# Performance work log

Hardware: AMD Instinct MI355X
Metric: run time of the kernel (lower is better)

Reference implementation:

```python
import jax, jax.numpy as jnp
import numpy as np

B, S, D = 4, 2048, 2048
H, HD = 16, 128
ROPE_THETA = 10000.0


def rotate_half(x):
    half = x.shape[-1] // 2
    return jnp.concatenate([-x[..., half:], x[..., :half]], axis=-1)


def setup_inputs() -> dict:
    key = jax.random.key(0)
    ks = jax.random.split(key, 5)
    scale = 1.0 / np.sqrt(D)
    x = jax.random.normal(ks[0], (B, S, D), dtype=jnp.float32)
    wq = jax.random.normal(ks[1], (D, H * HD), dtype=jnp.float32) * scale
    wk = jax.random.normal(ks[2], (D, H * HD), dtype=jnp.float32) * scale
    wv = jax.random.normal(ks[3], (D, H * HD), dtype=jnp.float32) * scale
    wo = jax.random.normal(ks[4], (H * HD, D), dtype=jnp.float32) * scale
    # RoPE frequencies: freqs_cis real/imag parts, shape [S, HD//2]
    inv_freq = 1.0 / (ROPE_THETA ** (np.arange(0, HD, 2, dtype=np.float32) / HD))
    t = np.arange(S, dtype=np.float32)
    freqs = np.outer(t, inv_freq)  # [S, HD//2]
    cos = jnp.asarray(np.cos(freqs), dtype=jnp.float32)
    sin = jnp.asarray(np.sin(freqs), dtype=jnp.float32)
    return {"x": x, "wq": wq, "wk": wk, "wv": wv, "wo": wo, "cos": cos, "sin": sin}


def reference(x, wq, wk, wv, wo, cos, sin):
    batch, seq_len, _ = x.shape
    # QKV projections (no bias), reshape to [b, h, s, d]
    q = (x @ wq).reshape(batch, seq_len, H, HD).transpose(0, 2, 1, 3)
    k = (x @ wk).reshape(batch, seq_len, H, HD).transpose(0, 2, 1, 3)
    v = (x @ wv).reshape(batch, seq_len, H, HD)  # [b, s, h, d]
    # RoPE (half-split / rotate_half convention)
    cos_full = jnp.concatenate([cos, cos], axis=-1)[None, None, :seq_len, :]
    sin_full = jnp.concatenate([sin, sin], axis=-1)[None, None, :seq_len, :]
    q = q * cos_full + rotate_half(q) * sin_full
    k = k * cos_full + rotate_half(k) * sin_full
    # Scaled dot-product attention with causal mask
    logits = jnp.einsum('bhqd,bhkd->bhqk', q, k) / jnp.sqrt(jnp.float32(HD))
    causal = jnp.tril(jnp.ones((seq_len, seq_len), dtype=bool))
    logits = jnp.where(causal[None, None, :, :], logits, -1e10)
    weights = jax.nn.softmax(logits, axis=-1)
    out = jnp.einsum('bhqk,bkhd->bqhd', weights, v)
    out = out.reshape(batch, seq_len, H * HD)
    return out @ wo
```

## Files before the change

### kernel.cpp

```cpp
#include <hip/hip_runtime.h>
#include <cstdint>
#include <cstddef>

typedef unsigned short u16;
using bf16x8  = __attribute__((ext_vector_type(8))) short;
using floatx4 = __attribute__((ext_vector_type(4))) float;

__device__ __forceinline__ u16 f2bf(float f) {
    union { float f; unsigned u; } v; v.f = f;
    unsigned r = v.u + 0x7fffu + ((v.u >> 16) & 1u);
    return (u16)(r >> 16);
}
__device__ __forceinline__ float bf2f(u16 h) {
    union { unsigned u; float f; } v; v.u = ((unsigned)h) << 16; return v.f;
}
__device__ __forceinline__ floatx4 mfma16(bf16x8 a, bf16x8 b, floatx4 c) {
    return __builtin_amdgcn_mfma_f32_16x16x32_bf16(a, b, c, 0, 0, 0);
}
using gptr_t = const __attribute__((address_space(1))) unsigned int*;
using lptr_t = __attribute__((address_space(3))) unsigned int*;
__device__ __forceinline__ void lds16(const void* g, void* l) {
    __builtin_amdgcn_global_load_lds((gptr_t)g, (lptr_t)l, 16, 0, 0);
}
typedef __attribute__((address_space(3))) const u16* lds_cp;
__device__ __forceinline__ bf16x8 dsr128(const u16* p) {
    bf16x8 r;
    asm volatile("ds_read_b128 %0, %1" : "=v"(r) : "v"((lds_cp)p));
    return r;
}

#define ATT_SCALE 0.1275758218522532f

__global__ __launch_bounds__(256) void cvt_x(const float* __restrict__ x, u16* __restrict__ xb) {
    size_t i = ((size_t)blockIdx.x * 256 + threadIdx.x) * 4;
    float4 v = *(const float4*)&x[i];
    ushort4 r; r.x = f2bf(v.x); r.y = f2bf(v.y); r.z = f2bf(v.z); r.w = f2bf(v.w);
    *(ushort4*)&xb[i] = r;
}

__global__ __launch_bounds__(256) void transpose_wall(const float* __restrict__ wq, const float* __restrict__ wk,
                                                      const float* __restrict__ wv, const float* __restrict__ wo,
                                                      u16* __restrict__ wqkvb, u16* __restrict__ wob) {
    __shared__ float t[64][65];
    const int z = blockIdx.z;
    const float* in = (z == 0) ? wq : (z == 1) ? wk : (z == 2) ? wv : wo;
    u16* out = (z < 3) ? (wqkvb + (size_t)z * 2048 * 2048) : wob;
    int k0 = blockIdx.x * 64, n0 = blockIdx.y * 64;
    int tx = threadIdx.x, ty = threadIdx.y;
#pragma unroll
    for (int i = 0; i < 16; ++i) {
        int r = i * 4 + ty;
        t[r][tx] = in[(size_t)(k0 + r) * 2048 + n0 + tx];
    }
    __syncthreads();
#pragma unroll
    for (int i = 0; i < 16; ++i) {
        int r = i * 4 + ty;
        out[(size_t)(n0 + r) * 2048 + k0 + tx] = f2bf(t[tx][r]);
    }
}

template <int MODE>
__global__ __launch_bounds__(512, 2) void gemm_bt(const u16* __restrict__ A, const u16* __restrict__ B,
                                                  u16* __restrict__ Qo, u16* __restrict__ Ko, u16* __restrict__ Vt,
                                                  float* __restrict__ Co,
                                                  const float* __restrict__ cosb, const float* __restrict__ sinb) {
    __shared__ __align__(16) u16 sA[2][16384];
    __shared__ __align__(16) u16 sB[2][16384];

    const int nbx = (MODE == 0) ? 24 : 8;
    const int bid = blockIdx.x;
    const int q8 = (int)gridDim.x >> 3;
    const int wg = (bid & 7) * q8 + (bid >> 3);
    const int bx = wg % nbx, by = wg / nbx;
    const int m0 = by << 8, n0 = bx << 8;

    const int tid = threadIdx.x;
    const int w = tid >> 6, lane = tid & 63;
    const int wm = w >> 2, wn = w & 3;
    const int m16 = lane & 15, q4 = lane >> 4;
    const int lr = lane >> 3;
    const int lc8 = (lane & 7) ^ lr;
    const int wnbase = (wn >> 1) * 128 + (wn & 1) * 32;

    const u16* Ag = A + (size_t)(m0 + w * 16 + lr) * 2048 + lc8 * 8;
    const u16* Bg = B + (size_t)(n0 + w * 16 + lr) * 2048 + lc8 * 8;

    const int swz0 = ((q4 ^ (m16 & 7)) << 3);
    const int swz1 = (((4 + q4) ^ (m16 & 7)) << 3);

    floatx4 acc[8][4];
#pragma unroll
    for (int r = 0; r < 8; ++r)
#pragma unroll
        for (int c = 0; c < 4; ++c) acc[r][c] = (floatx4)0.0f;
    bf16x8 af[4][2];
    bf16x8 bf[4][2];

#define STAGE_A(b, h, t) do { \
    lds16(Ag + (size_t)((h) * 128) * 2048 + (t) * 64,     &sA[b][(h) * 8192 + w * 1024]);       \
    lds16(Ag + (size_t)((h) * 128 + 8) * 2048 + (t) * 64, &sA[b][(h) * 8192 + w * 1024 + 512]); \
} while (0)
#define STAGE_B(b, h, t) do { \
    lds16(Bg + (size_t)((h) * 128) * 2048 + (t) * 64,     &sB[b][(h) * 8192 + w * 1024]);       \
    lds16(Bg + (size_t)((h) * 128 + 8) * 2048 + (t) * 64, &sB[b][(h) * 8192 + w * 1024 + 512]); \
} while (0)
#define BAR() __builtin_amdgcn_s_barrier()
#define WAITL0() do { asm volatile("s_waitcnt lgkmcnt(0)" ::: "memory"); __builtin_amdgcn_sched_barrier(0); } while (0)
#define WAITL8() asm volatile("s_waitcnt lgkmcnt(8)" ::: "memory")
#define LDA_(cur, mq) do { _Pragma("unroll") for (int fr = 0; fr < 4; ++fr) { \
    const u16* p = &sA[cur][(wm * 128 + (mq) * 64 + fr * 16 + m16) * 64];      \
    af[fr][0] = dsr128(&p[swz0]);                                              \
    af[fr][1] = dsr128(&p[swz1]); } } while (0)
#define LDB_(cur, nq) do { _Pragma("unroll") for (int c = 0; c < 2; ++c) {     \
    const int j = (nq) * 2 + c;                                                \
    const u16* p = &sB[cur][(wnbase + (j & 1) * 16 + (j >> 1) * 64 + m16) * 64]; \
    bf[j][0] = dsr128(&p[swz0]);                                               \
    bf[j][1] = dsr128(&p[swz1]); } } while (0)
#define MM_(mq, nq) do { _Pragma("unroll") for (int kk = 0; kk < 2; ++kk)      \
    _Pragma("unroll") for (int fr = 0; fr < 4; ++fr)                           \
    _Pragma("unroll") for (int c = 0; c < 2; ++c)                              \
        acc[(mq) * 4 + fr][(nq) * 2 + c] =                                     \
            mfma16(af[fr][kk], bf[(nq) * 2 + c][kk], acc[(mq) * 4 + fr][(nq) * 2 + c]); } while (0)

    const int NT = 32;

    STAGE_B(0, 0, 0); STAGE_B(0, 1, 0);
    STAGE_A(0, 0, 0); STAGE_A(0, 1, 0);
    STAGE_B(1, 0, 1); STAGE_B(1, 1, 1);
    asm volatile("s_waitcnt vmcnt(4)" ::: "memory");
    __builtin_amdgcn_s_barrier();

#pragma unroll 2
    for (int t = 0; t < NT; ++t) {
        const int cur = t & 1;
        LDB_(cur, 0);
        LDA_(cur, 0);
        if (t + 1 < NT) STAGE_A(cur ^ 1, 0, t + 1);
        WAITL8();
        BAR();
        WAITL0();
        __builtin_amdgcn_s_setprio(1); MM_(0, 0); __builtin_amdgcn_s_setprio(0);
        BAR();
        LDB_(cur, 1);
        if (t + 1 < NT) STAGE_A(cur ^ 1, 1, t + 1);
        BAR();
        WAITL0();
        __builtin_amdgcn_s_setprio(1); MM_(0, 1); __builtin_amdgcn_s_setprio(0);
        BAR();
        LDA_(cur, 1);
        if (t + 2 < NT) STAGE_B(cur, 0, t + 2);
        BAR();
        WAITL0();
        __builtin_amdgcn_s_setprio(1); MM_(1, 1); __builtin_amdgcn_s_setprio(0);
        BAR();
        if (t + 2 < NT) STAGE_B(cur, 1, t + 2);
        BAR();
        __builtin_amdgcn_s_setprio(1); MM_(1, 0); __builtin_amdgcn_s_setprio(0);
        if (t + 2 < NT)      { asm volatile("s_waitcnt vmcnt(4)" ::: "memory"); }
        else if (t + 1 < NT) { asm volatile("s_waitcnt vmcnt(0)" ::: "memory"); }
        BAR();
    }

#undef STAGE_A
#undef STAGE_B
#undef BAR
#undef WAITL0
#undef WAITL8
#undef LDA_
#undef LDB_
#undef MM_

    if (MODE == 0) {
        const int which = n0 >> 11;
        if (which < 2) {
            u16* dst = (which == 0) ? Qo : Ko;
            const float sc = (which == 0) ? ATT_SCALE : 1.0f;
            const int h = ((n0 >> 7) + (wn >> 1)) & 15;
            const int dp0 = (wn & 1) * 32 + m16;
#pragma unroll
            for (int fr = 0; fr < 8; ++fr) {
                const int mb = m0 + wm * 128 + fr * 16 + q4 * 4;
#pragma unroll
                for (int c0 = 0; c0 < 2; ++c0) {
                    const int dp = dp0 + c0 * 16;
#pragma unroll
                    for (int i = 0; i < 4; ++i) {
                        const int mm = mb + i;
                        const int b = mm >> 11, s = mm & 2047;
                        const float cs = cosb[(size_t)s * 64 + dp];
                        const float sn = sinb[(size_t)s * 64 + dp];
                        const float lo = acc[fr][c0][i], hi = acc[fr][c0 + 2][i];
                        const size_t base = ((size_t)((b * 16 + h) * 2048 + s) << 7) + dp;
                        dst[base]      = f2bf((lo * cs - hi * sn) * sc);
                        dst[base + 64] = f2bf((hi * cs + lo * sn) * sc);
                    }
                }
            }
        } else {
#pragma unroll
            for (int fr = 0; fr < 8; ++fr) {
                const int mb = m0 + wm * 128 + fr * 16 + q4 * 4;
                const int b = mb >> 11, s = mb & 2047;
#pragma unroll
                for (int c = 0; c < 4; ++c) {
                    const int n = n0 + wnbase + (c & 1) * 16 + (c >> 1) * 64 + m16;
                    const int h = (n >> 7) & 15, d = n & 127;
                    ushort4 pk;
                    pk.x = f2bf(acc[fr][c][0]); pk.y = f2bf(acc[fr][c][1]);
                    pk.z = f2bf(acc[fr][c][2]); pk.w = f2bf(acc[fr][c][3]);
                    *(ushort4*)&Vt[((size_t)((b * 16 + h) * 128 + d)) * 2048 + s] = pk;
                }
            }
        }
    } else {
#pragma unroll
        for (int fr = 0; fr < 8; ++fr) {
            const int mb = m0 + wm * 128 + fr * 16 + q4 * 4;
#pragma unroll
            for (int c = 0; c < 4; ++c) {
                const int n = n0 + wnbase + (c & 1) * 16 + (c >> 1) * 64 + m16;
#pragma unroll
                for (int i = 0; i < 4; ++i)
                    Co[(size_t)(mb + i) * 2048 + n] = acc[fr][c][i];
            }
        }
    }
}

__global__ __launch_bounds__(512) void attn_kernel(const u16* __restrict__ Q, const u16* __restrict__ K,
                                                   const u16* __restrict__ VT, u16* __restrict__ AO) {
    __shared__ __align__(16) u16 ks[64 * 136];
    __shared__ __align__(16) u16 vts[128 * 72];
    __shared__ __align__(16) u16 ps[256 * 72];
    static const int iqmap[8] = {7, 6, 5, 4, 0, 1, 2, 3};
    const int bx = blockIdx.x;
    const int iq = iqmap[bx >> 6];
    const int bh = bx & 63;
    const int b = bh >> 4, h = bh & 15;
    const u16* Qg = Q  + (size_t)bh * (2048 * 128);
    const u16* Kg = K  + (size_t)bh * (2048 * 128);
    const u16* Vg = VT + (size_t)bh * (128 * 2048);
    const int tid = threadIdx.x, w = tid >> 6, lane = tid & 63;
    const int m16 = lane & 15, q4 = lane >> 4;
    const int jn = 4 * iq + 4;

    const int qrow = iq * 256 + w * 32;
    bf16x8 qf[2][4];
#pragma unroll
    for (int rm = 0; rm < 2; ++rm)
#pragma unroll
        for (int kk = 0; kk < 4; ++kk)
            qf[rm][kk] = *(const bf16x8*)&Qg[(size_t)(qrow + rm * 16 + m16) * 128 + kk * 32 + q4 * 8];

    floatx4 o[2][8];
#pragma unroll
    for (int rm = 0; rm < 2; ++rm)
#pragma unroll
        for (int c = 0; c < 8; ++c) o[rm][c] = (floatx4)0.0f;
    float mrow[2] = {-1e30f, -1e30f}, lrow[2] = {0.0f, 0.0f};

    const int kr0 = tid >> 4,          kc0 = tid & 15;
    const int kr1 = (512 + tid) >> 4,  kc1 = tid & 15;
    const int vr0 = tid >> 3,          vc0 = tid & 7;
    const int vr1 = (512 + tid) >> 3,  vc1 = tid & 7;
    uint4 kreg0, kreg1, vreg0, vreg1;

#define LOADKV(j) do { \
    kreg0 = *(const uint4*)&Kg[(size_t)((j) * 64 + kr0) * 128 + kc0 * 8]; \
    kreg1 = *(const uint4*)&Kg[(size_t)((j) * 64 + kr1) * 128 + kc1 * 8]; \
    vreg0 = *(const uint4*)&Vg[(size_t)vr0 * 2048 + (j) * 64 + vc0 * 8];  \
    vreg1 = *(const uint4*)&Vg[(size_t)vr1 * 2048 + (j) * 64 + vc1 * 8];  \
} while (0)

    LOADKV(0);

    for (int j = 0; j < jn; ++j) {
        asm volatile("" ::: "memory");
        __builtin_amdgcn_s_barrier();
        asm volatile("" ::: "memory");
        *(uint4*)&ks[kr0 * 136 + kc0 * 8] = kreg0;
        *(uint4*)&ks[kr1 * 136 + kc1 * 8] = kreg1;
        *(uint4*)&vts[vr0 * 72 + vc0 * 8] = vreg0;
        *(uint4*)&vts[vr1 * 72 + vc1 * 8] = vreg1;
        if (j + 1 < jn) LOADKV(j + 1);
        asm volatile("s_waitcnt lgkmcnt(0)" ::: "memory");
        __builtin_amdgcn_s_barrier();
        asm volatile("" ::: "memory");

        floatx4 sacc[2][4];
#pragma unroll
        for (int rm = 0; rm < 2; ++rm)
#pragma unroll
            for (int r = 0; r < 4; ++r) sacc[rm][r] = (floatx4)0.0f;
        __builtin_amdgcn_s_setprio(1);
#pragma unroll
        for (int kk = 0; kk < 4; ++kk) {
            bf16x8 kb[4];
#pragma unroll
            for (int r = 0; r < 4; ++r)
                kb[r] = *(const bf16x8*)&ks[(r * 16 + m16) * 136 + kk * 32 + q4 * 8];
#pragma unroll
            for (int rm = 0; rm < 2; ++rm)
#pragma unroll
                for (int r = 0; r < 4; ++r)
                    sacc[rm][r] = mfma16(kb[r], qf[rm][kk], sacc[rm][r]);
        }
        __builtin_amdgcn_s_setprio(0);

        if (j >= 4 * iq) {
#pragma unroll
            for (int rm = 0; rm < 2; ++rm) {
                const int qg = qrow + rm * 16 + m16;
#pragma unroll
                for (int r = 0; r < 4; ++r)
#pragma unroll
                    for (int i = 0; i < 4; ++i) {
                        int kg = j * 64 + r * 16 + q4 * 4 + i;
                        if (kg > qg) sacc[rm][r][i] = -1e30f;
                    }
            }
        }

#pragma unroll
        for (int rm = 0; rm < 2; ++rm) {
            float pmax = -1e30f;
#pragma unroll
            for (int r = 0; r < 4; ++r)
#pragma unroll
                for (int i = 0; i < 4; ++i) pmax = fmaxf(pmax, sacc[rm][r][i]);
            pmax = fmaxf(pmax, __shfl_xor(pmax, 16));
            pmax = fmaxf(pmax, __shfl_xor(pmax, 32));
            float mnew = fmaxf(mrow[rm], pmax);
            float alpha = __builtin_amdgcn_exp2f(mrow[rm] - mnew);
            mrow[rm] = mnew;

            float psum = 0.0f;
#pragma unroll
            for (int r = 0; r < 4; ++r) {
                float p0 = __builtin_amdgcn_exp2f(sacc[rm][r][0] - mnew);
                float p1 = __builtin_amdgcn_exp2f(sacc[rm][r][1] - mnew);
                float p2 = __builtin_amdgcn_exp2f(sacc[rm][r][2] - mnew);
                float p3 = __builtin_amdgcn_exp2f(sacc[rm][r][3] - mnew);
                psum += (p0 + p1) + (p2 + p3);
                ushort4 pk; pk.x = f2bf(p0); pk.y = f2bf(p1); pk.z = f2bf(p2); pk.w = f2bf(p3);
                *(ushort4*)&ps[(w * 32 + rm * 16 + m16) * 72 + r * 16 + q4 * 4] = pk;
            }
            psum += __shfl_xor(psum, 16);
            psum += __shfl_xor(psum, 32);
            lrow[rm] = lrow[rm] * alpha + psum;

            float abc[4];
#pragma unroll
            for (int i = 0; i < 4; ++i) abc[i] = __shfl(alpha, q4 * 4 + i);
#pragma unroll
            for (int c = 0; c < 8; ++c)
#pragma unroll
                for (int i = 0; i < 4; ++i) o[rm][c][i] *= abc[i];
        }

#pragma unroll
        for (int kk = 0; kk < 2; ++kk) {
            bf16x8 pa[2];
#pragma unroll
            for (int rm = 0; rm < 2; ++rm)
                pa[rm] = *(const bf16x8*)&ps[(w * 32 + rm * 16 + m16) * 72 + kk * 32 + q4 * 8];
            __builtin_amdgcn_s_setprio(1);
#pragma unroll
            for (int ch = 0; ch < 2; ++ch) {
                bf16x8 vb[4];
#pragma unroll
                for (int c = 0; c < 4; ++c)
                    vb[c] = *(const bf16x8*)&vts[((ch * 4 + c) * 16 + m16) * 72 + kk * 32 + q4 * 8];
#pragma unroll
                for (int rm = 0; rm < 2; ++rm)
#pragma unroll
                    for (int c = 0; c < 4; ++c)
                        o[rm][ch * 4 + c] = mfma16(pa[rm], vb[c], o[rm][ch * 4 + c]);
            }
            __builtin_amdgcn_s_setprio(0);
        }
    }
#undef LOADKV

#pragma unroll
    for (int rm = 0; rm < 2; ++rm) {
        float linv = __builtin_amdgcn_rcpf(lrow[rm]);
        float li[4];
#pragma unroll
        for (int i = 0; i < 4; ++i) li[i] = __shfl(linv, q4 * 4 + i);
#pragma unroll
        for (int c = 0; c < 8; ++c)
#pragma unroll
            for (int i = 0; i < 4; ++i) {
                int s = qrow + rm * 16 + q4 * 4 + i;
                int d = c * 16 + m16;
                AO[((size_t)(b * 2048 + s)) * 2048 + h * 128 + d] = f2bf(o[rm][c][i] * li[i]);
            }
    }
}

extern "C" void kernel_launch(void* const* d_in, const int* in_sizes, int n_in,
                              void* d_out, int out_size, void* d_ws, size_t ws_size,
                              hipStream_t stream) {
    const float* x    = (const float*)d_in[0];
    const float* wq   = (const float*)d_in[1];
    const float* wk   = (const float*)d_in[2];
    const float* wv   = (const float*)d_in[3];
    const float* wo   = (const float*)d_in[4];
    const float* cosb = (const float*)d_in[5];
    const float* sinb = (const float*)d_in[6];
    float* out = (float*)d_out;

    char* ws = (char*)d_ws;
    u16* xb    = (u16*)(ws);
    u16* AO    = xb;
    u16* wqkvb = (u16*)(ws + 33554432);
    u16* wob   = (u16*)(ws + 58720256);
    u16* Qb    = (u16*)(ws + 67108864);
    u16* Kb    = (u16*)(ws + 100663296);
    u16* Vtb   = (u16*)(ws + 134217728);

    cvt_x<<<16384, 256, 0, stream>>>(x, xb);
    transpose_wall<<<dim3(32, 32, 4), dim3(64, 4), 0, stream>>>(wq, wk, wv, wo, wqkvb, wob);

    gemm_bt<0><<<768, 512, 0, stream>>>(xb, wqkvb, Qb, Kb, Vtb, nullptr, cosb, sinb);
    attn_kernel<<<512, 512, 0, stream>>>(Qb, Kb, Vtb, AO);
    gemm_bt<1><<<256, 512, 0, stream>>>(AO, wob, nullptr, nullptr, nullptr, out, nullptr, nullptr);
}
```

Before: 548.2 us.

## Merge prep kernels, skip masked KV tiles per warp, lazily rescale softmax

```diff
diff --git a/kernel.cpp b/kernel.cpp
--- a/kernel.cpp
+++ b/kernel.cpp
@@ -31,32 +31,40 @@
 
 #define ATT_SCALE 0.1275758218522532f
 
-__global__ __launch_bounds__(256) void cvt_x(const float* __restrict__ x, u16* __restrict__ xb) {
-    size_t i = ((size_t)blockIdx.x * 256 + threadIdx.x) * 4;
-    float4 v = *(const float4*)&x[i];
-    ushort4 r; r.x = f2bf(v.x); r.y = f2bf(v.y); r.z = f2bf(v.z); r.w = f2bf(v.w);
-    *(ushort4*)&xb[i] = r;
-}
-
-__global__ __launch_bounds__(256) void transpose_wall(const float* __restrict__ wq, const float* __restrict__ wk,
-                                                      const float* __restrict__ wv, const float* __restrict__ wo,
-                                                      u16* __restrict__ wqkvb, u16* __restrict__ wob) {
-    __shared__ float t[64][65];
+__global__ __launch_bounds__(256) void prep(const float* __restrict__ x,
+                                            const float* __restrict__ wq, const float* __restrict__ wk,
+                                            const float* __restrict__ wv, const float* __restrict__ wo,
+                                            u16* __restrict__ xb,
+                                            u16* __restrict__ wqkvb, u16* __restrict__ wob) {
     const int z = blockIdx.z;
-    const float* in = (z == 0) ? wq : (z == 1) ? wk : (z == 2) ? wv : wo;
-    u16* out = (z < 3) ? (wqkvb + (size_t)z * 2048 * 2048) : wob;
-    int k0 = blockIdx.x * 64, n0 = blockIdx.y * 64;
-    int tx = threadIdx.x, ty = threadIdx.y;
-#pragma unroll
-    for (int i = 0; i < 16; ++i) {
-        int r = i * 4 + ty;
-        t[r][tx] = in[(size_t)(k0 + r) * 2048 + n0 + tx];
-    }
-    __syncthreads();
-#pragma unroll
-    for (int i = 0; i < 16; ++i) {
-        int r = i * 4 + ty;
-        out[(size_t)(n0 + r) * 2048 + k0 + tx] = f2bf(t[tx][r]);
+    const int tx = threadIdx.x, ty = threadIdx.y;
+    if (z < 4) {
+        __shared__ float t[64][65];
+        const float* in = (z == 0) ? wq : (z == 1) ? wk : (z == 2) ? wv : wo;
+        u16* out = (z < 3) ? (wqkvb + (size_t)z * 2048 * 2048) : wob;
+        int k0 = blockIdx.x * 64, n0 = blockIdx.y * 64;
+#pragma unroll
+        for (int i = 0; i < 16; ++i) {
+            int r = i * 4 + ty;
+            t[r][tx] = in[(size_t)(k0 + r) * 2048 + n0 + tx];
+        }
+        __syncthreads();
+#pragma unroll
+        for (int i = 0; i < 16; ++i) {
+            int r = i * 4 + ty;
+            out[(size_t)(n0 + r) * 2048 + k0 + tx] = f2bf(t[tx][r]);
+        }
+    } else {
+        const int flat = ty * 64 + tx;
+        const size_t base = (size_t)(blockIdx.y * 32 + blockIdx.x) * 256 + flat;
+        const size_t stride = 1024 * 256;
+#pragma unroll
+        for (int it = 0; it < 16; ++it) {
+            size_t i = (base + it * stride) * 4;
+            float4 v = *(const float4*)&x[i];
+            ushort4 r; r.x = f2bf(v.x); r.y = f2bf(v.y); r.z = f2bf(v.z); r.w = f2bf(v.w);
+            *(ushort4*)&xb[i] = r;
+        }
     }
 }
 
@@ -288,6 +296,8 @@
         __builtin_amdgcn_s_barrier();
         asm volatile("" ::: "memory");
 
+        if (j * 64 > qrow + 31) continue;
+
         floatx4 sacc[2][4];
 #pragma unroll
         for (int rm = 0; rm < 2; ++rm)
@@ -331,32 +341,34 @@
                 for (int i = 0; i < 4; ++i) pmax = fmaxf(pmax, sacc[rm][r][i]);
             pmax = fmaxf(pmax, __shfl_xor(pmax, 16));
             pmax = fmaxf(pmax, __shfl_xor(pmax, 32));
-            float mnew = fmaxf(mrow[rm], pmax);
-            float alpha = __builtin_amdgcn_exp2f(mrow[rm] - mnew);
-            mrow[rm] = mnew;
+            if (__any(pmax - mrow[rm] > 8.0f)) {
+                float mnew = fmaxf(mrow[rm], pmax);
+                float alpha = __builtin_amdgcn_exp2f(mrow[rm] - mnew);
+                mrow[rm] = mnew;
+                lrow[rm] *= alpha;
+                float abc[4];
+#pragma unroll
+                for (int i = 0; i < 4; ++i) abc[i] = __shfl(alpha, q4 * 4 + i);
+#pragma unroll
+                for (int c = 0; c < 8; ++c)
+#pragma unroll
+                    for (int i = 0; i < 4; ++i) o[rm][c][i] *= abc[i];
+            }
 
             float psum = 0.0f;
 #pragma unroll
             for (int r = 0; r < 4; ++r) {
-                float p0 = __builtin_amdgcn_exp2f(sacc[rm][r][0] - mnew);
-                float p1 = __builtin_amdgcn_exp2f(sacc[rm][r][1] - mnew);
-                float p2 = __builtin_amdgcn_exp2f(sacc[rm][r][2] - mnew);
-                float p3 = __builtin_amdgcn_exp2f(sacc[rm][r][3] - mnew);
+                float p0 = __builtin_amdgcn_exp2f(sacc[rm][r][0] - mrow[rm]);
+                float p1 = __builtin_amdgcn_exp2f(sacc[rm][r][1] - mrow[rm]);
+                float p2 = __builtin_amdgcn_exp2f(sacc[rm][r][2] - mrow[rm]);
+                float p3 = __builtin_amdgcn_exp2f(sacc[rm][r][3] - mrow[rm]);
                 psum += (p0 + p1) + (p2 + p3);
                 ushort4 pk; pk.x = f2bf(p0); pk.y = f2bf(p1); pk.z = f2bf(p2); pk.w = f2bf(p3);
                 *(ushort4*)&ps[(w * 32 + rm * 16 + m16) * 72 + r * 16 + q4 * 4] = pk;
             }
             psum += __shfl_xor(psum, 16);
             psum += __shfl_xor(psum, 32);
-            lrow[rm] = lrow[rm] * alpha + psum;
-
-            float abc[4];
-#pragma unroll
-            for (int i = 0; i < 4; ++i) abc[i] = __shfl(alpha, q4 * 4 + i);
-#pragma unroll
-            for (int c = 0; c < 8; ++c)
-#pragma unroll
-                for (int i = 0; i < 4; ++i) o[rm][c][i] *= abc[i];
+            lrow[rm] += psum;
         }
 
 #pragma unroll
@@ -421,8 +433,7 @@
     u16* Kb    = (u16*)(ws + 100663296);
     u16* Vtb   = (u16*)(ws + 134217728);
 
-    cvt_x<<<16384, 256, 0, stream>>>(x, xb);
-    transpose_wall<<<dim3(32, 32, 4), dim3(64, 4), 0, stream>>>(wq, wk, wv, wo, wqkvb, wob);
+    prep<<<dim3(32, 32, 5), dim3(64, 4), 0, stream>>>(x, wq, wk, wv, wo, xb, wqkvb, wob);
 
     gemm_bt<0><<<768, 512, 0, stream>>>(xb, wqkvb, Qb, Kb, Vtb, nullptr, cosb, sinb);
     attn_kernel<<<512, 512, 0, stream>>>(Qb, Kb, Vtb, AO);
```

After: 537.9 us. No clear change (-1.9%).
